# Kernel optimization log

Hardware: AMD Instinct MI355X
Metric: run time of the kernel (lower is better)

The kernel has to match this reference:

```python
import jax, jax.numpy as jnp
import numpy as np

NUM_HEADS = 16
MAX_BATCH = 4
MAX_SEQ = 2048


def setup_inputs() -> dict:
    key = jax.random.key(0)
    ks = jax.random.split(key, 9)
    B, S, H = 4, 2048, 2048
    scale = 0.02
    hidden_state = jax.random.normal(ks[0], (B, S, H), dtype=jnp.float32)
    # causal mask (masked_fill where mask == 0), broadcastable over batch/heads
    mask = jnp.tril(jnp.ones((S, S), dtype=jnp.int32))[None, None]  # [1,1,S,S]
    Wq = jax.random.normal(ks[1], (H, H), dtype=jnp.float32) * scale
    Wk = jax.random.normal(ks[2], (H, H), dtype=jnp.float32) * scale
    Wv = jax.random.normal(ks[3], (H, H), dtype=jnp.float32) * scale
    Wo = jax.random.normal(ks[4], (H, H), dtype=jnp.float32) * scale
    bq = jax.random.normal(ks[5], (H,), dtype=jnp.float32) * scale
    bk = jax.random.normal(ks[6], (H,), dtype=jnp.float32) * scale
    bv = jax.random.normal(ks[7], (H,), dtype=jnp.float32) * scale
    bo = jax.random.normal(ks[8], (H,), dtype=jnp.float32) * scale
    return {"hidden_state": hidden_state, "mask": mask,
            "Wq": Wq, "bq": bq, "Wk": Wk, "bk": bk,
            "Wv": Wv, "bv": bv, "Wo": Wo, "bo": bo,
            "start_pos": 0}


def reference(hidden_state, mask, Wq, bq, Wk, bk, Wv, bv, Wo, bo, start_pos):
    B, S, H = hidden_state.shape
    nh = NUM_HEADS
    hd = H // nh
    # qkv projections (nn.Linear: x @ W.T + b)
    q = (hidden_state @ Wq.T + bq).reshape(B, S, nh, hd)
    k = (hidden_state @ Wk.T + bk).reshape(B, S, nh, hd)
    v = (hidden_state @ Wv.T + bv).reshape(B, S, nh, hd)
    # KV-cache append (zeros-initialized buffer, write [start_pos:start_pos+S])
    cache_k = jnp.zeros((MAX_BATCH, MAX_SEQ, nh, hd), dtype=q.dtype)
    cache_v = jnp.zeros((MAX_BATCH, MAX_SEQ, nh, hd), dtype=q.dtype)
    cache_k = jax.lax.dynamic_update_slice(cache_k, k, (0, start_pos, 0, 0))
    cache_v = jax.lax.dynamic_update_slice(cache_v, v, (0, start_pos, 0, 0))
    total = start_pos + S
    key = cache_k[:B, :total]   # [B, total, nh, hd]
    value = cache_v[:B, :total]
    # scores: [B, nh, S, total]
    scores = jnp.einsum('bqhd,bkhd->bhqk', q, key) / jnp.sqrt(jnp.float32(hd))
    scores = jnp.where(mask == 0, -jnp.inf, scores)
    probs = jax.nn.softmax(scores, axis=-1)
    out = jnp.einsum('bhqk,bkhd->bqhd', probs, value).reshape(B, S, H)
    return out @ Wo.T + bo
```

## Files before the change

kernel.cpp:

```cpp
#include <hip/hip_runtime.h>
#include <hip/hip_bf16.h>
#include <stdint.h>

#define S_LEN 2048
#define HDIM  2048
#define NH    16
#define HD    128
#define BATCH 4

typedef __attribute__((ext_vector_type(8))) short bf16x8;
typedef __attribute__((ext_vector_type(4))) float f32x4;
typedef __attribute__((ext_vector_type(4))) float float4v;
typedef __attribute__((ext_vector_type(4))) unsigned short u16x4;

__device__ __forceinline__ void gload_lds16(const void* g, void* l) {
  __builtin_amdgcn_global_load_lds(
      (const __attribute__((address_space(1))) unsigned int*)g,
      (__attribute__((address_space(3))) unsigned int*)l,
      16, 0, 0);
}

__device__ __forceinline__ unsigned short f2bf(float x) {
  __hip_bfloat16 b = __float2bfloat16(x);
  return *reinterpret_cast<unsigned short*>(&b);
}

__global__ __launch_bounds__(256) void cvt_kernel(const float* __restrict__ in,
                                                  unsigned short* __restrict__ out,
                                                  int n4) {
  int stride = gridDim.x * blockDim.x;
  for (int i = blockIdx.x * blockDim.x + threadIdx.x; i < n4; i += stride) {
    float4v v = *(const float4v*)(in + (size_t)i * 4);
    u16x4 o;
    o.x = f2bf(v.x); o.y = f2bf(v.y); o.z = f2bf(v.z); o.w = f2bf(v.w);
    *(u16x4*)(out + (size_t)i * 4) = o;
  }
}

__global__ __launch_bounds__(256) void cvt4_kernel(
    const float* __restrict__ w0, const float* __restrict__ w1,
    const float* __restrict__ w2, const float* __restrict__ w3,
    unsigned short* __restrict__ o0, unsigned short* __restrict__ o1,
    unsigned short* __restrict__ o2, unsigned short* __restrict__ o3,
    int n4) {
  const int y = blockIdx.y;
  const float* in = (y == 0) ? w0 : (y == 1) ? w1 : (y == 2) ? w2 : w3;
  unsigned short* out = (y == 0) ? o0 : (y == 1) ? o1 : (y == 2) ? o2 : o3;
  int stride = gridDim.x * blockDim.x;
  for (int i = blockIdx.x * blockDim.x + threadIdx.x; i < n4; i += stride) {
    float4v v = *(const float4v*)(in + (size_t)i * 4);
    u16x4 o;
    o.x = f2bf(v.x); o.y = f2bf(v.y); o.z = f2bf(v.z); o.w = f2bf(v.w);
    *(u16x4*)(out + (size_t)i * 4) = o;
  }
}


#define G8_VMW(N) asm volatile("s_waitcnt vmcnt(" #N ")" ::: "memory")
#define G8_BAR1() do { __builtin_amdgcn_sched_barrier(0); __builtin_amdgcn_s_barrier(); \
  asm volatile("s_waitcnt lgkmcnt(0)" ::: "memory"); __builtin_amdgcn_sched_barrier(0); } while (0)
#define G8_BAR2() do { __builtin_amdgcn_sched_barrier(0); __builtin_amdgcn_s_barrier(); \
  __builtin_amdgcn_sched_barrier(0); } while (0)

#define G8_STAGE(ISB, BUF, HALF, KT) do {                                          \
  int kt_ = (KT); if (kt_ > nkt1) kt_ = nkt1;                                      \
  const char* gs_ = ((ISB) ? Bg : Ag) +                                            \
      (size_t)(((ISB) ? bn : bm) * 256 + (HALF) * 128 + w * 16) * (size_t)K2 +     \
      (size_t)kt_ * 128;                                                           \
  char* ld_ = lds + (BUF) * 65536 + (ISB) * 32768 + ((HALF) * 128 + w * 16) * 128; \
  gload_lds16(gs_ + sLn, ld_);                                                     \
  gload_lds16(gs_ + 8 * (size_t)K2 + sLn, ld_ + 1024);                             \
} while (0)

#define G8_RDA(BUF, MI0) do {                                                      \
  _Pragma("unroll") for (int mi = 0; mi < 4; ++mi)                                 \
  _Pragma("unroll") for (int kk = 0; kk < 2; ++kk)                                 \
    a[mi][kk] = *(const bf16x8*)(lds + (BUF) * 65536 +                             \
        (wm + ((MI0) + mi) * 16 + ln) * 128 + ((((kk << 2) + g) ^ ln7) << 4));     \
} while (0)

#define G8_RDB(BUF, NI0, BREG) do {                                                \
  _Pragma("unroll") for (int ni = 0; ni < 2; ++ni)                                 \
  _Pragma("unroll") for (int kk = 0; kk < 2; ++kk)                                 \
    BREG[ni][kk] = *(const bf16x8*)(lds + (BUF) * 65536 + 32768 +                  \
        (wn + ((NI0) + ni) * 16 + ln) * 128 + ((((kk << 2) + g) ^ ln7) << 4));     \
} while (0)

#define G8_MFMA(M0, N0, BREG) do {                                                 \
  __builtin_amdgcn_s_setprio(1);                                                   \
  _Pragma("unroll") for (int mi = 0; mi < 4; ++mi)                                 \
  _Pragma("unroll") for (int ni = 0; ni < 2; ++ni)                                 \
  _Pragma("unroll") for (int kk = 0; kk < 2; ++kk)                                 \
    acc[(M0) + mi][(N0) + ni] = __builtin_amdgcn_mfma_f32_16x16x32_bf16(           \
        a[mi][kk], BREG[ni][kk], acc[(M0) + mi][(N0) + ni], 0, 0, 0);              \
  __builtin_amdgcn_s_setprio(0);                                                   \
} while (0)

template<int OUTF32>
__global__ __launch_bounds__(512, 2) void gemm8(
    const __hip_bfloat16* __restrict__ A, const __hip_bfloat16* __restrict__ B,
    const float* __restrict__ bias, void* __restrict__ C,
    int M, int N, int K) {
  __shared__ char lds[131072];
  const int tid = threadIdx.x;
  const int w = tid >> 6;
  const int lane = tid & 63;
  const int g = lane >> 4;
  const int ln = lane & 15;
  const int ln7 = lane & 7;
  const int K2 = K * 2;
  const int nkt = K >> 6;
  const int nkt1 = nkt - 1;
  const int niter = nkt >> 1;

  const int NBN = N >> 8;
  const int nwg = (M >> 8) * NBN;
  const int cpx = nwg >> 3;
  const int bid = blockIdx.x;
  const int wg = (bid & 7) * cpx + (bid >> 3);
  const int bm = wg / NBN, bn = wg % NBN;

  const int wm = (w >> 2) * 128;
  const int wn = (w & 3) * 64;

  const char* Ag = (const char*)A;
  const char* Bg = (const char*)B;
  const size_t sLn = (size_t)(lane >> 3) * (size_t)K2 +
                     (size_t)(((lane & 7) ^ (lane >> 3)) << 4);

  f32x4 acc[8][4];
#pragma unroll
  for (int mi = 0; mi < 8; ++mi)
#pragma unroll
    for (int ni = 0; ni < 4; ++ni) acc[mi][ni] = (f32x4){0.f, 0.f, 0.f, 0.f};

  G8_STAGE(0, 0, 0, 0); G8_STAGE(0, 0, 1, 0);
  G8_STAGE(1, 0, 0, 0); G8_STAGE(1, 0, 1, 0);
  G8_STAGE(1, 1, 0, 1); G8_STAGE(1, 1, 1, 1);
  G8_VMW(4);
  G8_BAR2();

  for (int i = 0; i < niter; ++i) {
    const int v = 2 * i + 1, u2 = 2 * i + 2, v2 = 2 * i + 3;
    bf16x8 a[4][2], b0[2][2], b1[2][2];
    G8_RDA(0, 0); G8_RDB(0, 0, b0);
    G8_STAGE(0, 1, 0, v);
    G8_BAR1();
    G8_MFMA(0, 0, b0);
    G8_BAR2();
    G8_RDB(0, 2, b1);
    G8_STAGE(0, 1, 1, v);
    G8_BAR1();
    G8_MFMA(0, 2, b1);
    G8_BAR2();
    G8_RDA(0, 4);
    G8_STAGE(1, 0, 0, u2);
    G8_BAR1();
    G8_MFMA(4, 0, b0);
    G8_BAR2();
    G8_STAGE(1, 0, 1, u2);
    G8_VMW(4);
    G8_BAR1();
    G8_MFMA(4, 2, b1);
    G8_BAR2();
    G8_RDA(1, 0); G8_RDB(1, 0, b0);
    G8_STAGE(0, 0, 0, u2);
    G8_BAR1();
    G8_MFMA(0, 0, b0);
    G8_BAR2();
    G8_RDB(1, 2, b1);
    G8_STAGE(0, 0, 1, u2);
    G8_BAR1();
    G8_MFMA(0, 2, b1);
    G8_BAR2();
    G8_RDA(1, 4);
    G8_STAGE(1, 1, 0, v2);
    G8_BAR1();
    G8_MFMA(4, 0, b0);
    G8_BAR2();
    G8_STAGE(1, 1, 1, v2);
    G8_VMW(4);
    G8_BAR1();
    G8_MFMA(4, 2, b1);
    G8_BAR2();
  }

  G8_VMW(0);
#pragma unroll
  for (int ni = 0; ni < 4; ++ni) {
    const int col = bn * 256 + wn + ni * 16 + ln;
    const float bv = bias[col];
#pragma unroll
    for (int mi = 0; mi < 8; ++mi) {
      const int row0 = bm * 256 + wm + mi * 16 + g * 4;
#pragma unroll
      for (int r = 0; r < 4; ++r) {
        float val = acc[mi][ni][r] + bv;
        if (OUTF32)
          ((float*)C)[(size_t)(row0 + r) * N + col] = val;
        else
          ((__hip_bfloat16*)C)[(size_t)(row0 + r) * N + col] = __float2bfloat16(val);
      }
    }
  }
}

__global__ __launch_bounds__(256) void transpose_v(const __hip_bfloat16* __restrict__ V,
                                                   __hip_bfloat16* __restrict__ Vt) {
  __shared__ unsigned short t[64 * 132];
  const int tid = threadIdx.x;
  const int bh = blockIdx.y;
  const int b = bh >> 4, h = bh & 15;
  const int s0 = blockIdx.x * 64;
  const unsigned short* Vp = (const unsigned short*)V + (size_t)b * S_LEN * HDIM + h * HD;
#pragma unroll
  for (int i = 0; i < 4; i++) {
    int idx = i * 256 + tid;
    int s = idx >> 4, c = idx & 15;
    const uint64_t* src = (const uint64_t*)(Vp + (size_t)(s0 + s) * HDIM + c * 8);
    uint64_t v0 = src[0], v1 = src[1];
    uint64_t* dst = (uint64_t*)&t[s * 132 + c * 8];
    dst[0] = v0; dst[1] = v1;
  }
  __syncthreads();
  unsigned short* Vtp = (unsigned short*)Vt + (size_t)bh * HD * S_LEN;
#pragma unroll
  for (int i = 0; i < 8; i++) {
    int idx = i * 256 + tid;
    int d = idx >> 4, sc = idx & 15;
    u16x4 vv;
    vv.x = t[(sc * 4 + 0) * 132 + d];
    vv.y = t[(sc * 4 + 1) * 132 + d];
    vv.z = t[(sc * 4 + 2) * 132 + d];
    vv.w = t[(sc * 4 + 3) * 132 + d];
    *(u16x4*)(Vtp + (size_t)d * S_LEN + s0 + sc * 4) = vv;
  }
}

#define SL2E 0.1275174465f
#define DEFER_THR 8.0f

__global__ __launch_bounds__(256, 2) void attn_kernel(
    const __hip_bfloat16* __restrict__ Q, const __hip_bfloat16* __restrict__ Kg,
    const __hip_bfloat16* __restrict__ Vt, __hip_bfloat16* __restrict__ O) {
  __shared__ char lds[49152];
  const int tid = threadIdx.x;
  const int w = tid >> 6;
  const int lane = tid & 63;
  const int g = lane >> 4;
  const int ln = lane & 15;
  const int bh = blockIdx.y;
  const int b = bh >> 4, h = bh & 15;

  const char* Qb = (const char*)Q + ((size_t)b * S_LEN * HDIM + h * HD) * 2;
  const char* Kb = (const char*)Kg + ((size_t)b * S_LEN * HDIM + h * HD) * 2;
  const char* Vb = (const char*)Vt + ((size_t)bh * HD * S_LEN) * 2;
  char* ldsK = lds;
  char* ldsV = lds + 16384;
  char* pw   = lds + 32768 + w * 4096;

  const int kr = lane >> 4;
  const int kc = lane & 15;
  const int vr = lane >> 3;
  const int vc = lane & 7;

  auto stage = [&](int kv0) {
#pragma unroll
    for (int i = 0; i < 4; i++) {
      int r = w * 16 + i * 4 + kr;
      gload_lds16(Kb + (size_t)(kv0 + r) * (HDIM * 2) + ((kc ^ (r & 7)) << 4),
                  ldsK + (w * 16 + i * 4) * 256);
    }
#pragma unroll
    for (int i = 0; i < 4; i++) {
      int r = w * 32 + i * 8 + vr;
      gload_lds16(Vb + (size_t)r * (S_LEN * 2) + (size_t)kv0 * 2 + ((vc ^ vr) << 4),
                  ldsV + (w * 32 + i * 8) * 128);
    }
  };

  for (int pass = 0; pass < 2; pass++) {
    const int qt = pass == 0 ? (15 - (int)blockIdx.x) : (int)blockIdx.x;
    const int q0 = qt * 128 + w * 32;

    bf16x8 qf[2][4];
#pragma unroll
    for (int qs = 0; qs < 2; qs++)
#pragma unroll
      for (int dc = 0; dc < 4; dc++)
        qf[qs][dc] = *(const bf16x8*)(Qb + (size_t)(q0 + qs * 16 + ln) * HDIM * 2 +
                                      (dc * 32 + g * 8) * 2);

    f32x4 o[2][8];
#pragma unroll
    for (int qs = 0; qs < 2; qs++)
#pragma unroll
      for (int ds = 0; ds < 8; ds++) o[qs][ds] = (f32x4){0.f, 0.f, 0.f, 0.f};
    float mrun[2][4], lrun[2][4];
#pragma unroll
    for (int qs = 0; qs < 2; qs++)
#pragma unroll
      for (int r = 0; r < 4; r++) { mrun[qs][r] = -__builtin_inff(); lrun[qs][r] = 0.f; }

    const int nt = 2 * qt + 2;
    __syncthreads();
    stage(0);
    __syncthreads();

    for (int t = 0; t < nt; t++) {
      const int kv0 = t * 64;

      if (kv0 <= q0 + 31) {
        f32x4 sa[2][4];
#pragma unroll
        for (int qs = 0; qs < 2; qs++)
#pragma unroll
          for (int ks = 0; ks < 4; ks++) sa[qs][ks] = (f32x4){0.f, 0.f, 0.f, 0.f};
#pragma unroll
        for (int dc = 0; dc < 4; dc++) {
          bf16x8 kf[4];
#pragma unroll
          for (int ks = 0; ks < 4; ks++)
            kf[ks] = *(const bf16x8*)(ldsK + (ks * 16 + ln) * 256 +
                                      (((dc * 4 + g) ^ (ln & 7)) << 4));
#pragma unroll
          for (int qs = 0; qs < 2; qs++)
#pragma unroll
            for (int ks = 0; ks < 4; ks++)
              sa[qs][ks] = __builtin_amdgcn_mfma_f32_16x16x32_bf16(qf[qs][dc], kf[ks], sa[qs][ks], 0, 0, 0);
        }
        const bool needmask = (kv0 + 63) > q0;
#pragma unroll
        for (int qs = 0; qs < 2; qs++)
#pragma unroll
          for (int ks = 0; ks < 4; ks++)
#pragma unroll
            for (int r = 0; r < 4; r++) {
              float s = sa[qs][ks][r] * SL2E;
              if (needmask && (kv0 + ks * 16 + ln) > (q0 + qs * 16 + g * 4 + r))
                s = -__builtin_inff();
              sa[qs][ks][r] = s;
            }
        float pmax[2][4];
#pragma unroll
        for (int qs = 0; qs < 2; qs++)
#pragma unroll
          for (int r = 0; r < 4; r++) {
            float mx = fmaxf(fmaxf(sa[qs][0][r], sa[qs][1][r]), fmaxf(sa[qs][2][r], sa[qs][3][r]));
            mx = fmaxf(mx, __shfl_xor(mx, 1));
            mx = fmaxf(mx, __shfl_xor(mx, 2));
            mx = fmaxf(mx, __shfl_xor(mx, 4));
            mx = fmaxf(mx, __shfl_xor(mx, 8));
            pmax[qs][r] = mx;
          }
        float dmin = 1e30f;
#pragma unroll
        for (int qs = 0; qs < 2; qs++)
#pragma unroll
          for (int r = 0; r < 4; r++)
            dmin = fminf(dmin, mrun[qs][r] + DEFER_THR - pmax[qs][r]);
        if (!__all(dmin >= 0.0f)) {
          float alpha[2][4];
#pragma unroll
          for (int qs = 0; qs < 2; qs++)
#pragma unroll
            for (int r = 0; r < 4; r++) {
              float mn = fmaxf(mrun[qs][r], pmax[qs][r]);
              alpha[qs][r] = exp2f(mrun[qs][r] - mn);
              mrun[qs][r] = mn;
              lrun[qs][r] *= alpha[qs][r];
            }
#pragma unroll
          for (int qs = 0; qs < 2; qs++)
#pragma unroll
            for (int ds = 0; ds < 8; ds++)
#pragma unroll
              for (int r = 0; r < 4; r++) o[qs][ds][r] *= alpha[qs][r];
        }
        float rsum[2][4];
#pragma unroll
        for (int qs = 0; qs < 2; qs++)
#pragma unroll
          for (int r = 0; r < 4; r++) rsum[qs][r] = 0.f;
#pragma unroll
        for (int qs = 0; qs < 2; qs++)
#pragma unroll
          for (int ks = 0; ks < 4; ks++)
#pragma unroll
            for (int r = 0; r < 4; r++) {
              float p = exp2f(sa[qs][ks][r] - mrun[qs][r]);
              sa[qs][ks][r] = p;
              rsum[qs][r] += p;
            }
#pragma unroll
        for (int qs = 0; qs < 2; qs++)
#pragma unroll
          for (int r = 0; r < 4; r++) {
            float rs = rsum[qs][r];
            rs += __shfl_xor(rs, 1);
            rs += __shfl_xor(rs, 2);
            rs += __shfl_xor(rs, 4);
            rs += __shfl_xor(rs, 8);
            lrun[qs][r] += rs;
          }
#pragma unroll
        for (int qs = 0; qs < 2; qs++)
#pragma unroll
          for (int ks = 0; ks < 4; ks++)
#pragma unroll
            for (int r = 0; r < 4; r++) {
              int row = qs * 16 + g * 4 + r;
              int key = ks * 16 + ln;
              *(__hip_bfloat16*)(pw + row * 128 + (((key >> 3) ^ (row & 7)) << 4) + (key & 7) * 2) =
                  __float2bfloat16(sa[qs][ks][r]);
            }
#pragma unroll
        for (int kk = 0; kk < 2; kk++) {
          bf16x8 pa[2];
#pragma unroll
          for (int qs = 0; qs < 2; qs++) {
            int row = qs * 16 + ln;
            pa[qs] = *(const bf16x8*)(pw + row * 128 + (((kk * 4 + g) ^ (row & 7)) << 4));
          }
#pragma unroll
          for (int ds = 0; ds < 8; ds++) {
            bf16x8 vf = *(const bf16x8*)(ldsV + (ds * 16 + ln) * 128 +
                                         (((kk * 4 + g) ^ (ln & 7)) << 4));
#pragma unroll
            for (int qs = 0; qs < 2; qs++)
              o[qs][ds] = __builtin_amdgcn_mfma_f32_16x16x32_bf16(pa[qs], vf, o[qs][ds], 0, 0, 0);
          }
        }
      }

      if (t + 1 < nt) {
        __syncthreads();
        stage(kv0 + 64);
        __syncthreads();
      }
    }
    float inv[2][4];
#pragma unroll
    for (int qs = 0; qs < 2; qs++)
#pragma unroll
      for (int r = 0; r < 4; r++) inv[qs][r] = 1.0f / lrun[qs][r];
    __hip_bfloat16* Ob = O + (size_t)b * S_LEN * HDIM + h * HD;
#pragma unroll
    for (int qs = 0; qs < 2; qs++)
#pragma unroll
      for (int ds = 0; ds < 8; ds++)
#pragma unroll
        for (int r = 0; r < 4; r++)
          Ob[(size_t)(q0 + qs * 16 + g * 4 + r) * HDIM + ds * 16 + ln] =
              __float2bfloat16(o[qs][ds][r] * inv[qs][r]);
  }
}

extern "C" void kernel_launch(void* const* d_in, const int* in_sizes, int n_in,
                              void* d_out, int out_size, void* d_ws, size_t ws_size,
                              hipStream_t stream) {
  const float* X  = (const float*)d_in[0];
  const float* Wq = (const float*)d_in[2];
  const float* bq = (const float*)d_in[3];
  const float* Wk = (const float*)d_in[4];
  const float* bk = (const float*)d_in[5];
  const float* Wv = (const float*)d_in[6];
  const float* bv = (const float*)d_in[7];
  const float* Wo = (const float*)d_in[8];
  const float* bo = (const float*)d_in[9];

  char* ws = (char*)d_ws;
  __hip_bfloat16* Xb   = (__hip_bfloat16*)(ws);
  __hip_bfloat16* Wqb  = (__hip_bfloat16*)(ws + 33554432);
  __hip_bfloat16* Wkb  = (__hip_bfloat16*)(ws + 41943040);
  __hip_bfloat16* Wvb  = (__hip_bfloat16*)(ws + 50331648);
  __hip_bfloat16* Wob  = (__hip_bfloat16*)(ws + 58720256);
  __hip_bfloat16* Qb   = (__hip_bfloat16*)(ws + 67108864);
  __hip_bfloat16* Kb   = (__hip_bfloat16*)(ws + 100663296);
  __hip_bfloat16* Vbuf = (__hip_bfloat16*)(ws + 134217728);
  __hip_bfloat16* Vtb  = (__hip_bfloat16*)(ws + 167772160);
  __hip_bfloat16* Ob   = Vbuf;

  cvt_kernel<<<2048, 256, 0, stream>>>(X,  (unsigned short*)Xb,  16777216 / 4);
  cvt4_kernel<<<dim3(512, 4), 256, 0, stream>>>(
      Wq, Wk, Wv, Wo,
      (unsigned short*)Wqb, (unsigned short*)Wkb,
      (unsigned short*)Wvb, (unsigned short*)Wob, 4194304 / 4);

  gemm8<0><<<256, 512, 0, stream>>>(Xb, Wqb, bq, Qb,   8192, 2048, 2048);
  gemm8<0><<<256, 512, 0, stream>>>(Xb, Wkb, bk, Kb,   8192, 2048, 2048);
  gemm8<0><<<256, 512, 0, stream>>>(Xb, Wvb, bv, Vbuf, 8192, 2048, 2048);

  transpose_v<<<dim3(32, 64), 256, 0, stream>>>(Vbuf, Vtb);

  attn_kernel<<<dim3(8, 64), 256, 0, stream>>>(Qb, Kb, Vtb, Ob);

  gemm8<1><<<256, 512, 0, stream>>>(Ob, Wob, bo, (float*)d_out, 8192, 2048, 2048);
}
```

Before: 484.8 us.

## Fuse V transpose and softmax scale into projection GEMM epilogues

The V projection GEMM gains a third output mode that writes its result directly in the per-head transposed [b,h,d,s] layout as packed 4-element stores, so the separate transpose_v kernel and its extra round trip through memory go away. The softmax scale (1/sqrt(hd)·log2e) is folded into the Q projection epilogue, which removes the per-element multiply in the attention kernel; the causal mask is now applied only when a tile needs it. In the attention kernel the first K/V tile is staged before the Q fragment loads, so the two overlap. The trade-offs are scattered 8-byte stores in the V GEMM epilogue and rounding Q to bf16 after scaling.

```diff
diff --git a/kernel.cpp b/kernel.cpp
--- a/kernel.cpp
+++ b/kernel.cpp
@@ -24,6 +24,8 @@
   __hip_bfloat16 b = __float2bfloat16(x);
   return *reinterpret_cast<unsigned short*>(&b);
 }
+
+#define SL2E 0.1275174465f
 
 __global__ __launch_bounds__(256) void cvt_kernel(const float* __restrict__ in,
                                                   unsigned short* __restrict__ out,
@@ -96,11 +98,11 @@
   __builtin_amdgcn_s_setprio(0);                                                   \
 } while (0)
 
-template<int OUTF32>
+template<int OUTMODE>
 __global__ __launch_bounds__(512, 2) void gemm8(
     const __hip_bfloat16* __restrict__ A, const __hip_bfloat16* __restrict__ B,
     const float* __restrict__ bias, void* __restrict__ C,
-    int M, int N, int K) {
+    int M, int N, int K, float scale) {
   __shared__ char lds[131072];
   const int tid = threadIdx.x;
   const int w = tid >> 6;
@@ -193,51 +195,29 @@
 #pragma unroll
     for (int mi = 0; mi < 8; ++mi) {
       const int row0 = bm * 256 + wm + mi * 16 + g * 4;
-#pragma unroll
-      for (int r = 0; r < 4; ++r) {
-        float val = acc[mi][ni][r] + bv;
-        if (OUTF32)
-          ((float*)C)[(size_t)(row0 + r) * N + col] = val;
-        else
-          ((__hip_bfloat16*)C)[(size_t)(row0 + r) * N + col] = __float2bfloat16(val);
+      if (OUTMODE == 2) {
+        const int h = col >> 7, d = col & 127;
+        const size_t base = ((size_t)((row0 >> 11) * NH + h) * HD + d) * S_LEN +
+                            (row0 & (S_LEN - 1));
+        u16x4 pk;
+#pragma unroll
+        for (int r = 0; r < 4; ++r)
+          pk[r] = f2bf((acc[mi][ni][r] + bv) * scale);
+        *(u16x4*)((unsigned short*)C + base) = pk;
+      } else {
+#pragma unroll
+        for (int r = 0; r < 4; ++r) {
+          float val = (acc[mi][ni][r] + bv) * scale;
+          if (OUTMODE == 1)
+            ((float*)C)[(size_t)(row0 + r) * N + col] = val;
+          else
+            ((__hip_bfloat16*)C)[(size_t)(row0 + r) * N + col] = __float2bfloat16(val);
+        }
       }
     }
   }
 }
 
-__global__ __launch_bounds__(256) void transpose_v(const __hip_bfloat16* __restrict__ V,
-                                                   __hip_bfloat16* __restrict__ Vt) {
-  __shared__ unsigned short t[64 * 132];
-  const int tid = threadIdx.x;
-  const int bh = blockIdx.y;
-  const int b = bh >> 4, h = bh & 15;
-  const int s0 = blockIdx.x * 64;
-  const unsigned short* Vp = (const unsigned short*)V + (size_t)b * S_LEN * HDIM + h * HD;
-#pragma unroll
-  for (int i = 0; i < 4; i++) {
-    int idx = i * 256 + tid;
-    int s = idx >> 4, c = idx & 15;
-    const uint64_t* src = (const uint64_t*)(Vp + (size_t)(s0 + s) * HDIM + c * 8);
-    uint64_t v0 = src[0], v1 = src[1];
-    uint64_t* dst = (uint64_t*)&t[s * 132 + c * 8];
-    dst[0] = v0; dst[1] = v1;
-  }
-  __syncthreads();
-  unsigned short* Vtp = (unsigned short*)Vt + (size_t)bh * HD * S_LEN;
-#pragma unroll
-  for (int i = 0; i < 8; i++) {
-    int idx = i * 256 + tid;
-    int d = idx >> 4, sc = idx & 15;
-    u16x4 vv;
-    vv.x = t[(sc * 4 + 0) * 132 + d];
-    vv.y = t[(sc * 4 + 1) * 132 + d];
-    vv.z = t[(sc * 4 + 2) * 132 + d];
-    vv.w = t[(sc * 4 + 3) * 132 + d];
-    *(u16x4*)(Vtp + (size_t)d * S_LEN + s0 + sc * 4) = vv;
-  }
-}
-
-#define SL2E 0.1275174465f
 #define DEFER_THR 8.0f
 
 __global__ __launch_bounds__(256, 2) void attn_kernel(
@@ -283,6 +263,10 @@
     const int qt = pass == 0 ? (15 - (int)blockIdx.x) : (int)blockIdx.x;
     const int q0 = qt * 128 + w * 32;
 
+    const int nt = 2 * qt + 2;
+    __syncthreads();
+    stage(0);
+
     bf16x8 qf[2][4];
 #pragma unroll
     for (int qs = 0; qs < 2; qs++)
@@ -302,9 +286,6 @@
 #pragma unroll
       for (int r = 0; r < 4; r++) { mrun[qs][r] = -__builtin_inff(); lrun[qs][r] = 0.f; }
 
-    const int nt = 2 * qt + 2;
-    __syncthreads();
-    stage(0);
     __syncthreads();
 
     for (int t = 0; t < nt; t++) {
@@ -330,17 +311,16 @@
               sa[qs][ks] = __builtin_amdgcn_mfma_f32_16x16x32_bf16(qf[qs][dc], kf[ks], sa[qs][ks], 0, 0, 0);
         }
         const bool needmask = (kv0 + 63) > q0;
-#pragma unroll
-        for (int qs = 0; qs < 2; qs++)
-#pragma unroll
-          for (int ks = 0; ks < 4; ks++)
-#pragma unroll
-            for (int r = 0; r < 4; r++) {
-              float s = sa[qs][ks][r] * SL2E;
-              if (needmask && (kv0 + ks * 16 + ln) > (q0 + qs * 16 + g * 4 + r))
-                s = -__builtin_inff();
-              sa[qs][ks][r] = s;
-            }
+        if (needmask) {
+#pragma unroll
+          for (int qs = 0; qs < 2; qs++)
+#pragma unroll
+            for (int ks = 0; ks < 4; ks++)
+#pragma unroll
+              for (int r = 0; r < 4; r++)
+                if ((kv0 + ks * 16 + ln) > (q0 + qs * 16 + g * 4 + r))
+                  sa[qs][ks][r] = -__builtin_inff();
+        }
         float pmax[2][4];
 #pragma unroll
         for (int qs = 0; qs < 2; qs++)
@@ -477,9 +457,8 @@
   __hip_bfloat16* Wob  = (__hip_bfloat16*)(ws + 58720256);
   __hip_bfloat16* Qb   = (__hip_bfloat16*)(ws + 67108864);
   __hip_bfloat16* Kb   = (__hip_bfloat16*)(ws + 100663296);
-  __hip_bfloat16* Vbuf = (__hip_bfloat16*)(ws + 134217728);
+  __hip_bfloat16* Ob   = (__hip_bfloat16*)(ws + 134217728);
   __hip_bfloat16* Vtb  = (__hip_bfloat16*)(ws + 167772160);
-  __hip_bfloat16* Ob   = Vbuf;
 
   cvt_kernel<<<2048, 256, 0, stream>>>(X,  (unsigned short*)Xb,  16777216 / 4);
   cvt4_kernel<<<dim3(512, 4), 256, 0, stream>>>(
@@ -487,13 +466,11 @@
       (unsigned short*)Wqb, (unsigned short*)Wkb,
       (unsigned short*)Wvb, (unsigned short*)Wob, 4194304 / 4);
 
-  gemm8<0><<<256, 512, 0, stream>>>(Xb, Wqb, bq, Qb,   8192, 2048, 2048);
-  gemm8<0><<<256, 512, 0, stream>>>(Xb, Wkb, bk, Kb,   8192, 2048, 2048);
-  gemm8<0><<<256, 512, 0, stream>>>(Xb, Wvb, bv, Vbuf, 8192, 2048, 2048);
-
-  transpose_v<<<dim3(32, 64), 256, 0, stream>>>(Vbuf, Vtb);
+  gemm8<0><<<256, 512, 0, stream>>>(Xb, Wqb, bq, Qb,  8192, 2048, 2048, SL2E);
+  gemm8<0><<<256, 512, 0, stream>>>(Xb, Wkb, bk, Kb,  8192, 2048, 2048, 1.0f);
+  gemm8<2><<<256, 512, 0, stream>>>(Xb, Wvb, bv, Vtb, 8192, 2048, 2048, 1.0f);
 
   attn_kernel<<<dim3(8, 64), 256, 0, stream>>>(Qb, Kb, Vtb, Ob);
 
-  gemm8<1><<<256, 512, 0, stream>>>(Ob, Wob, bo, (float*)d_out, 8192, 2048, 2048);
-}
+  gemm8<1><<<256, 512, 0, stream>>>(Ob, Wob, bo, (float*)d_out, 8192, 2048, 2048, 1.0f);
+}
```

Result: faster. 450.9 us (-7.0%).
